# Performance work log

Hardware: AMD Instinct MI355X
Metric: run time of the kernel (lower is better)

## Reference

```python
import jax, jax.numpy as jnp
import numpy as np

T_MAX = 1.0


def _mlp(x, W1, b1, W2, b2):
    # 2-layer tanh MLP: state -> hidden -> state
    return jnp.tanh(x @ W1 + b1) @ W2 + b2


def setup_inputs() -> dict:
    key = jax.random.key(0)
    ks = jax.random.split(key, 10)
    B, S, Hd, N = 128, 256, 512, 1000
    sc_s = 1.0 / np.sqrt(S)
    sc_h = 1.0 / np.sqrt(Hd)
    return {
        "x0": jax.random.normal(ks[0], (B, S), jnp.float32),
        "Wd1": jax.random.normal(ks[1], (S, Hd), jnp.float32) * sc_s,
        "bd1": jnp.zeros((Hd,), jnp.float32),
        "Wd2": jax.random.normal(ks[2], (Hd, S), jnp.float32) * sc_h,
        "bd2": jnp.zeros((S,), jnp.float32),
        "Ws1": jax.random.normal(ks[3], (S, Hd), jnp.float32) * sc_s,
        "bs1": jnp.zeros((Hd,), jnp.float32),
        "Ws2": jax.random.normal(ks[4], (Hd, S), jnp.float32) * sc_h,
        "bs2": jnp.zeros((S,), jnp.float32),
        "raw_h": jnp.array(0.0, jnp.float32),  # logit(0.5) -> H = 0.5
        # Davies-Harte fGn with H=0.5 is iid N(0,1); step-major layout for scan
        "fgn": jax.random.normal(ks[5], (N, B, S), jnp.float32),
        "n_steps": N,
    }


def reference(x0, Wd1, bd1, Wd2, bd2, Ws1, bs1, Ws2, bs2, raw_h, fgn, n_steps):
    dt = T_MAX / n_steps
    H = jax.nn.sigmoid(raw_h) * 0.98 + 0.01
    noise_inc = fgn * (dt ** H)  # [n_steps, B, S]

    def step(xt, noise):
        drift = _mlp(xt, Wd1, bd1, Wd2, bd2) * dt
        diffusion = _mlp(xt, Ws1, bs1, Ws2, bs2)
        xt = xt + drift + diffusion * noise
        return xt, xt

    _, traj = jax.lax.scan(step, x0, noise_inc)  # [n_steps, B, S]
    # trajectory = stack([x0, x1, ..., xN], dim=1) -> [B, n_steps+1, S]
    return jnp.concatenate([x0[:, None, :], jnp.swapaxes(traj, 0, 1)], axis=1)
```

## Files before the change

kernel.cpp:

```cpp
#include <hip/hip_runtime.h>
#include <hip/hip_bf16.h>
#include <stdint.h>


typedef __attribute__((ext_vector_type(8))) short bf16x8;
typedef __attribute__((ext_vector_type(4))) float f32x4;
typedef __attribute__((ext_vector_type(4))) unsigned short u16x4;

#define MFMA16(a, b, c) __builtin_amdgcn_mfma_f32_16x16x32_bf16((a), (b), (c), 0, 0, 0)

__device__ __forceinline__ unsigned short f2bf(float f) {
  union { float f; uint32_t u; } v; v.f = f;
  return (unsigned short)((v.u + 0x7fffu + ((v.u >> 16) & 1u)) >> 16);
}

__device__ __forceinline__ float fast_tanh(float z) {
  float az = __builtin_fabsf(z);
  float e = __expf(-2.0f * az);
  float r = (1.0f - e) * __builtin_amdgcn_rcpf(1.0f + e);
  return z < 0.0f ? -r : r;
}

__device__ __forceinline__ void store_wt_i(int* p, int v) {
  asm volatile("global_store_dword %0, %1, off sc0 sc1" :: "v"(p), "v"(v) : "memory");
}
__device__ __forceinline__ int load_wt_i(const int* p) {
  int v;
  asm volatile("global_load_dword %0, %1, off sc0 sc1\n\ts_waitcnt vmcnt(0)"
               : "=&v"(v) : "v"(p) : "memory");
  return v;
}

__device__ __forceinline__ void store_dev_f(float* p, float v) {
  asm volatile("global_store_dword %0, %1, off sc1" :: "v"(p), "v"(v) : "memory");
}

__global__ __launch_bounds__(256, 1) void fsde_kernel(
    const float* __restrict__ x0,
    const float* __restrict__ Wd1, const float* __restrict__ bd1,
    const float* __restrict__ Wd2, const float* __restrict__ bd2,
    const float* __restrict__ Ws1, const float* __restrict__ bs1,
    const float* __restrict__ Ws2, const float* __restrict__ bs2,
    const float* __restrict__ rawh,
    const float* __restrict__ fgn,
    const int* __restrict__ nsp,
    float* __restrict__ out,
    float* __restrict__ part,
    int* __restrict__ flags)
{
  __shared__ __align__(16) unsigned short Xs[16 * 264];
  __shared__ __align__(16) unsigned short Hs[16 * 136];
  __shared__ __align__(16) unsigned short STG[8704];
  __shared__ float B1[128];

  const int tid = threadIdx.x;
  const int lane = tid & 63;
  const int wv = tid >> 6;
  const int q = lane >> 4;
  const int cl = lane & 15;

  const int bid = blockIdx.x;
  const int c = (bid & 7) * 4 + ((bid >> 3) >> 3);
  const int j = (bid >> 3) & 7;

  const int NS = nsp[0];
  const float dt = 1.0f / (float)NS;
  const float Hh = 0.98f / (1.0f + expf(-rawh[0])) + 0.01f;
  const float nsc = expf(Hh * logf(dt));

  const float* W1g = (j < 4) ? Wd1 : Ws1;
  const float* W2g = (j < 4) ? Wd2 : Ws2;
  const float* b1g = (j < 4) ? bd1 : bs1;
  const int jj = (j & 3) * 128;

  bf16x8 w1f[2][8];
  for (int wc = 0; wc < 4; ++wc) {
    __syncthreads();
    for (int idx = tid; idx < 32 * 256; idx += 256) {
      int n = idx & 31, k = idx >> 5;
      STG[n * 264 + k] = f2bf(W1g[k * 512 + jj + wc * 32 + n]);
    }
    __syncthreads();
    if (wv == wc) {
#pragma unroll
      for (int i = 0; i < 2; ++i)
#pragma unroll
        for (int kt = 0; kt < 8; ++kt)
          w1f[i][kt] = *(const bf16x8*)&STG[(i * 16 + cl) * 264 + kt * 32 + q * 8];
    }
  }
  bf16x8 w2f[4][4];
  for (int wc = 0; wc < 4; ++wc) {
    __syncthreads();
    for (int idx = tid; idx < 64 * 128; idx += 256) {
      int n = idx & 63, k = idx >> 6;
      STG[n * 136 + k] = f2bf(W2g[(jj + k) * 256 + wc * 64 + n]);
    }
    __syncthreads();
    if (wv == wc) {
#pragma unroll
      for (int i = 0; i < 4; ++i)
#pragma unroll
        for (int kt = 0; kt < 4; ++kt)
          w2f[i][kt] = *(const bf16x8*)&STG[(i * 16 + cl) * 136 + kt * 32 + q * 8];
    }
  }

  if (tid < 128) B1[tid] = b1g[jj + tid];
  for (int idx = tid; idx < 12 * 264; idx += 256) Xs[4 * 264 + idx] = 0;

  const int ub = tid >> 6;
  const int us4 = tid & 63;
  const int us = us4 * 4;
  const int grow = 4 * c + ub;

  f32x4 xr = *(const f32x4*)(x0 + grow * 256 + us);
  f32x4 b2d = *(const f32x4*)(bd2 + us);
  f32x4 b2s = *(const f32x4*)(bs2 + us);

  {
    u16x4 xu;
#pragma unroll
    for (int i2 = 0; i2 < 4; ++i2) xu[i2] = f2bf(xr[i2]);
    *(u16x4*)&Xs[ub * 264 + us] = xu;
  }
  float* trow = out + (size_t)grow * (size_t)(NS + 1) * 256 + us;
  if (j == 0) *(f32x4*)trow = xr;

  __syncthreads();

  for (int t = 0; t < NS; ++t) {
    f32x4 nf = *(const f32x4*)(fgn + ((size_t)t * 128 + grow) * 256 + us);

    f32x4 acc0 = {0.f, 0.f, 0.f, 0.f}, acc1 = {0.f, 0.f, 0.f, 0.f};
#pragma unroll
    for (int kt = 0; kt < 8; ++kt) {
      bf16x8 a = *(const bf16x8*)&Xs[cl * 264 + kt * 32 + q * 8];
      acc0 = MFMA16(a, w1f[0][kt], acc0);
      acc1 = MFMA16(a, w1f[1][kt], acc1);
    }
#pragma unroll
    for (int i = 0; i < 2; ++i) {
      int col = (wv * 2 + i) * 16 + cl;
      float bb = B1[col];
      f32x4 v = i ? acc1 : acc0;
#pragma unroll
      for (int r = 0; r < 4; ++r)
        Hs[(q * 4 + r) * 136 + col] = f2bf(fast_tanh(v[r] + bb));
    }
    __syncthreads();

    f32x4 pacc[4] = {{0.f,0.f,0.f,0.f},{0.f,0.f,0.f,0.f},{0.f,0.f,0.f,0.f},{0.f,0.f,0.f,0.f}};
#pragma unroll
    for (int kt = 0; kt < 4; ++kt) {
      bf16x8 a = *(const bf16x8*)&Hs[cl * 136 + kt * 32 + q * 8];
#pragma unroll
      for (int i = 0; i < 4; ++i) pacc[i] = MFMA16(a, w2f[i][kt], pacc[i]);
    }

    float* pbase = part + ((size_t)((t & 1) * 32 + c) * 8 + j) * 1024;
    if (q == 0) {
#pragma unroll
      for (int i = 0; i < 4; ++i) {
        int col = (wv * 4 + i) * 16 + cl;
#pragma unroll
        for (int r = 0; r < 4; ++r) store_dev_f(pbase + r * 256 + col, pacc[i][r]);
      }
    }
    asm volatile("s_waitcnt vmcnt(0)" ::: "memory");
    __syncthreads();
    if (tid == 0) store_wt_i(flags + c * 8 + j, t + 1);
    if (tid < 8) {
      const int* fp = flags + c * 8 + tid;
      while (load_wt_i(fp) < t + 1) {}
    }
    __syncthreads();

    f32x4 p0, p1, p2, p3, p4, p5, p6, p7;
    {
      const uint32_t voff = (uint32_t)(ub * 1024 + us4 * 16);
      const float* gb = part + ((size_t)((t & 1) * 32 + c) * 8) * 1024;
      asm volatile(
          "global_load_dwordx4 %0, %8, %9 sc1\n\t"
          "global_load_dwordx4 %1, %8, %10 sc1\n\t"
          "global_load_dwordx4 %2, %8, %11 sc1\n\t"
          "global_load_dwordx4 %3, %8, %12 sc1\n\t"
          "global_load_dwordx4 %4, %8, %13 sc1\n\t"
          "global_load_dwordx4 %5, %8, %14 sc1\n\t"
          "global_load_dwordx4 %6, %8, %15 sc1\n\t"
          "global_load_dwordx4 %7, %8, %16 sc1\n\t"
          "s_waitcnt vmcnt(0)"
          : "=&v"(p0), "=&v"(p1), "=&v"(p2), "=&v"(p3),
            "=&v"(p4), "=&v"(p5), "=&v"(p6), "=&v"(p7)
          : "v"(voff),
            "s"(gb), "s"(gb + 1024), "s"(gb + 2048), "s"(gb + 3072),
            "s"(gb + 4096), "s"(gb + 5120), "s"(gb + 6144), "s"(gb + 7168)
          : "memory");
    }
    f32x4 dsum = p0 + p1 + p2 + p3;
    f32x4 ssum = p4 + p5 + p6 + p7;
#pragma unroll
    for (int i2 = 0; i2 < 4; ++i2)
      xr[i2] += (dsum[i2] + b2d[i2]) * dt + (ssum[i2] + b2s[i2]) * (nf[i2] * nsc);

    {
      u16x4 xu;
#pragma unroll
      for (int i2 = 0; i2 < 4; ++i2) xu[i2] = f2bf(xr[i2]);
      *(u16x4*)&Xs[ub * 264 + us] = xu;
    }
    if (j == 0) *(f32x4*)(trow + (size_t)(t + 1) * 256) = xr;
    __syncthreads();
  }
}

extern "C" void kernel_launch(void* const* d_in, const int* in_sizes, int n_in,
                              void* d_out, int out_size, void* d_ws, size_t ws_size,
                              hipStream_t stream) {
  const float* x0  = (const float*)d_in[0];
  const float* Wd1 = (const float*)d_in[1];
  const float* bd1 = (const float*)d_in[2];
  const float* Wd2 = (const float*)d_in[3];
  const float* bd2 = (const float*)d_in[4];
  const float* Ws1 = (const float*)d_in[5];
  const float* bs1 = (const float*)d_in[6];
  const float* Ws2 = (const float*)d_in[7];
  const float* bs2 = (const float*)d_in[8];
  const float* rawh = (const float*)d_in[9];
  const float* fgn = (const float*)d_in[10];
  const int* nsp = (const int*)d_in[11];
  float* out = (float*)d_out;

  float* part = (float*)d_ws;
  int* flags = (int*)((char*)d_ws + (size_t)(2 * 1024 * 1024));

  hipMemsetAsync(flags, 0, 32 * 8 * sizeof(int), stream);

  fsde_kernel<<<dim3(256), dim3(256), 0, stream>>>(
      x0, Wd1, bd1, Wd2, bd2, Ws1, bs1, Ws2, bs2, rawh, fgn, nsp, out, part, flags);
}
```

Baseline: 3.035 ms.

## Replace flag-based inter-block barrier with step-tagged partial sums polled directly

Each partial-sum value is now stored together with its step index as a dwordx2 pair, and consumers poll the partial buffer until every tag matches the current step. This removes the separate flag write, the block-wide syncthreads and waits around it, and the flag-polling round trip on every step. The cost is twice the partial-buffer traffic and retry loads of the full data. The workspace is not cleared, so stale tags from a previous launch could match and be read as valid.

New measurement: 4.308 ms. 42.0% more time.

```diff
diff --git a/kernel.cpp b/kernel.cpp
--- a/kernel.cpp
+++ b/kernel.cpp
@@ -6,6 +6,8 @@
 typedef __attribute__((ext_vector_type(8))) short bf16x8;
 typedef __attribute__((ext_vector_type(4))) float f32x4;
 typedef __attribute__((ext_vector_type(4))) unsigned short u16x4;
+typedef __attribute__((ext_vector_type(2))) unsigned int u32x2;
+typedef __attribute__((ext_vector_type(4))) unsigned int u32x4;
 
 #define MFMA16(a, b, c) __builtin_amdgcn_mfma_f32_16x16x32_bf16((a), (b), (c), 0, 0, 0)
 
@@ -19,20 +21,6 @@
   float e = __expf(-2.0f * az);
   float r = (1.0f - e) * __builtin_amdgcn_rcpf(1.0f + e);
   return z < 0.0f ? -r : r;
-}
-
-__device__ __forceinline__ void store_wt_i(int* p, int v) {
-  asm volatile("global_store_dword %0, %1, off sc0 sc1" :: "v"(p), "v"(v) : "memory");
-}
-__device__ __forceinline__ int load_wt_i(const int* p) {
-  int v;
-  asm volatile("global_load_dword %0, %1, off sc0 sc1\n\ts_waitcnt vmcnt(0)"
-               : "=&v"(v) : "v"(p) : "memory");
-  return v;
-}
-
-__device__ __forceinline__ void store_dev_f(float* p, float v) {
-  asm volatile("global_store_dword %0, %1, off sc1" :: "v"(p), "v"(v) : "memory");
 }
 
 __global__ __launch_bounds__(256, 1) void fsde_kernel(
@@ -45,8 +33,7 @@
     const float* __restrict__ fgn,
     const int* __restrict__ nsp,
     float* __restrict__ out,
-    float* __restrict__ part,
-    int* __restrict__ flags)
+    float* __restrict__ part)
 {
   __shared__ __align__(16) unsigned short Xs[16 * 264];
   __shared__ __align__(16) unsigned short Hs[16 * 136];
@@ -158,47 +145,91 @@
       for (int i = 0; i < 4; ++i) pacc[i] = MFMA16(a, w2f[i][kt], pacc[i]);
     }
 
-    float* pbase = part + ((size_t)((t & 1) * 32 + c) * 8 + j) * 1024;
+    float* pbase = part + ((size_t)((t & 1) * 32 + c) * 8 + j) * 2048;
     if (q == 0) {
 #pragma unroll
       for (int i = 0; i < 4; ++i) {
         int col = (wv * 4 + i) * 16 + cl;
 #pragma unroll
-        for (int r = 0; r < 4; ++r) store_dev_f(pbase + r * 256 + col, pacc[i][r]);
+        for (int r = 0; r < 4; ++r) {
+          u32x2 pr;
+          pr[0] = __float_as_uint(pacc[i][r]);
+          pr[1] = (unsigned)(t + 1);
+          asm volatile("global_store_dwordx2 %0, %1, off sc0 sc1"
+                       :: "v"(pbase + (size_t)(r * 256 + col) * 2), "v"(pr)
+                       : "memory");
+        }
       }
     }
-    asm volatile("s_waitcnt vmcnt(0)" ::: "memory");
-    __syncthreads();
-    if (tid == 0) store_wt_i(flags + c * 8 + j, t + 1);
-    if (tid < 8) {
-      const int* fp = flags + c * 8 + tid;
-      while (load_wt_i(fp) < t + 1) {}
-    }
-    __syncthreads();
-
-    f32x4 p0, p1, p2, p3, p4, p5, p6, p7;
+
+    u32x4 g0, g1, g2, g3, g4, g5, g6, g7, g8, g9, g10, g11, g12, g13, g14, g15;
     {
-      const uint32_t voff = (uint32_t)(ub * 1024 + us4 * 16);
-      const float* gb = part + ((size_t)((t & 1) * 32 + c) * 8) * 1024;
-      asm volatile(
-          "global_load_dwordx4 %0, %8, %9 sc1\n\t"
-          "global_load_dwordx4 %1, %8, %10 sc1\n\t"
-          "global_load_dwordx4 %2, %8, %11 sc1\n\t"
-          "global_load_dwordx4 %3, %8, %12 sc1\n\t"
-          "global_load_dwordx4 %4, %8, %13 sc1\n\t"
-          "global_load_dwordx4 %5, %8, %14 sc1\n\t"
-          "global_load_dwordx4 %6, %8, %15 sc1\n\t"
-          "global_load_dwordx4 %7, %8, %16 sc1\n\t"
-          "s_waitcnt vmcnt(0)"
-          : "=&v"(p0), "=&v"(p1), "=&v"(p2), "=&v"(p3),
-            "=&v"(p4), "=&v"(p5), "=&v"(p6), "=&v"(p7)
-          : "v"(voff),
-            "s"(gb), "s"(gb + 1024), "s"(gb + 2048), "s"(gb + 3072),
-            "s"(gb + 4096), "s"(gb + 5120), "s"(gb + 6144), "s"(gb + 7168)
-          : "memory");
-    }
-    f32x4 dsum = p0 + p1 + p2 + p3;
-    f32x4 ssum = p4 + p5 + p6 + p7;
+      const uint64_t voff = (uint64_t)(ub * 2048 + us4 * 32);
+      const float* gb = part + ((size_t)((t & 1) * 32 + c) * 8) * 2048;
+      const uint64_t a0 = (uint64_t)gb + voff;
+      const uint64_t a1 = a0 + 8192 * 1;
+      const uint64_t a2 = a0 + 8192 * 2;
+      const uint64_t a3 = a0 + 8192 * 3;
+      const uint64_t a4 = a0 + 8192 * 4;
+      const uint64_t a5 = a0 + 8192 * 5;
+      const uint64_t a6 = a0 + 8192 * 6;
+      const uint64_t a7 = a0 + 8192 * 7;
+      const unsigned tg = (unsigned)(t + 1);
+      int ok;
+      do {
+        asm volatile(
+            "global_load_dwordx4 %0, %16, off sc0 sc1\n\t"
+            "global_load_dwordx4 %1, %16, off offset:16 sc0 sc1\n\t"
+            "global_load_dwordx4 %2, %17, off sc0 sc1\n\t"
+            "global_load_dwordx4 %3, %17, off offset:16 sc0 sc1\n\t"
+            "global_load_dwordx4 %4, %18, off sc0 sc1\n\t"
+            "global_load_dwordx4 %5, %18, off offset:16 sc0 sc1\n\t"
+            "global_load_dwordx4 %6, %19, off sc0 sc1\n\t"
+            "global_load_dwordx4 %7, %19, off offset:16 sc0 sc1\n\t"
+            "global_load_dwordx4 %8, %20, off sc0 sc1\n\t"
+            "global_load_dwordx4 %9, %20, off offset:16 sc0 sc1\n\t"
+            "global_load_dwordx4 %10, %21, off sc0 sc1\n\t"
+            "global_load_dwordx4 %11, %21, off offset:16 sc0 sc1\n\t"
+            "global_load_dwordx4 %12, %22, off sc0 sc1\n\t"
+            "global_load_dwordx4 %13, %22, off offset:16 sc0 sc1\n\t"
+            "global_load_dwordx4 %14, %23, off sc0 sc1\n\t"
+            "global_load_dwordx4 %15, %23, off offset:16 sc0 sc1\n\t"
+            "s_waitcnt vmcnt(0)"
+            : "=&v"(g0), "=&v"(g1), "=&v"(g2), "=&v"(g3),
+              "=&v"(g4), "=&v"(g5), "=&v"(g6), "=&v"(g7),
+              "=&v"(g8), "=&v"(g9), "=&v"(g10), "=&v"(g11),
+              "=&v"(g12), "=&v"(g13), "=&v"(g14), "=&v"(g15)
+            : "v"(a0), "v"(a1), "v"(a2), "v"(a3),
+              "v"(a4), "v"(a5), "v"(a6), "v"(a7)
+            : "memory");
+        ok = (g0[1] == tg) & (g0[3] == tg) & (g1[1] == tg) & (g1[3] == tg) &
+             (g2[1] == tg) & (g2[3] == tg) & (g3[1] == tg) & (g3[3] == tg) &
+             (g4[1] == tg) & (g4[3] == tg) & (g5[1] == tg) & (g5[3] == tg) &
+             (g6[1] == tg) & (g6[3] == tg) & (g7[1] == tg) & (g7[3] == tg) &
+             (g8[1] == tg) & (g8[3] == tg) & (g9[1] == tg) & (g9[3] == tg) &
+             (g10[1] == tg) & (g10[3] == tg) & (g11[1] == tg) & (g11[3] == tg) &
+             (g12[1] == tg) & (g12[3] == tg) & (g13[1] == tg) & (g13[3] == tg) &
+             (g14[1] == tg) & (g14[3] == tg) & (g15[1] == tg) & (g15[3] == tg);
+      } while (__builtin_expect(!ok, 0));
+    }
+    f32x4 dsum, ssum;
+    dsum[0] = __uint_as_float(g0[0]) + __uint_as_float(g2[0]) +
+              __uint_as_float(g4[0]) + __uint_as_float(g6[0]);
+    dsum[1] = __uint_as_float(g0[2]) + __uint_as_float(g2[2]) +
+              __uint_as_float(g4[2]) + __uint_as_float(g6[2]);
+    dsum[2] = __uint_as_float(g1[0]) + __uint_as_float(g3[0]) +
+              __uint_as_float(g5[0]) + __uint_as_float(g7[0]);
+    dsum[3] = __uint_as_float(g1[2]) + __uint_as_float(g3[2]) +
+              __uint_as_float(g5[2]) + __uint_as_float(g7[2]);
+    ssum[0] = __uint_as_float(g8[0]) + __uint_as_float(g10[0]) +
+              __uint_as_float(g12[0]) + __uint_as_float(g14[0]);
+    ssum[1] = __uint_as_float(g8[2]) + __uint_as_float(g10[2]) +
+              __uint_as_float(g12[2]) + __uint_as_float(g14[2]);
+    ssum[2] = __uint_as_float(g9[0]) + __uint_as_float(g11[0]) +
+              __uint_as_float(g13[0]) + __uint_as_float(g15[0]);
+    ssum[3] = __uint_as_float(g9[2]) + __uint_as_float(g11[2]) +
+              __uint_as_float(g13[2]) + __uint_as_float(g15[2]);
+
 #pragma unroll
     for (int i2 = 0; i2 < 4; ++i2)
       xr[i2] += (dsum[i2] + b2d[i2]) * dt + (ssum[i2] + b2s[i2]) * (nf[i2] * nsc);
@@ -232,10 +263,7 @@
   float* out = (float*)d_out;
 
   float* part = (float*)d_ws;
-  int* flags = (int*)((char*)d_ws + (size_t)(2 * 1024 * 1024));
-
-  hipMemsetAsync(flags, 0, 32 * 8 * sizeof(int), stream);
 
   fsde_kernel<<<dim3(256), dim3(256), 0, stream>>>(
-      x0, Wd1, bd1, Wd2, bd2, Ws1, bs1, Ws2, bs2, rawh, fgn, nsp, out, part, flags);
-}
+      x0, Wd1, bd1, Wd2, bd2, Ws1, bs1, Ws2, bs2, rawh, fgn, nsp, out, part);
+}
```
